# Performance work log

Hardware: AMD Instinct MI355X
Metric: run time of the kernel (lower is better)

Reference implementation:

```python
import math
import jax, jax.numpy as jnp
import numpy as np

HALF_PI = math.pi / 2
TWOR_SCALE = 1.0 / math.log(2.0)
B, C, L, K = 32, 2, 262144, 4


def setup_inputs() -> dict:
    key = jax.random.key(0)
    ks = jax.random.split(key, 6)
    return {
        "input_signal": jax.random.normal(ks[0], (B, C, L), jnp.float32),
        "twoR": jax.random.normal(ks[1], (B, K), jnp.float32),
        "G": jax.random.normal(ks[2], (B, K), jnp.float32),
        "c_hp": jax.random.normal(ks[3], (B, K), jnp.float32),
        "c_bp": jax.random.normal(ks[4], (B, K), jnp.float32),
        "c_lp": jax.random.normal(ks[5], (B, K), jnp.float32),
    }


def get_biquad_coefficients(twoR, G, c_hp, c_bp, c_lp):
    # each arg: (B, K)
    G2 = G * G
    b0 = c_hp + c_bp * G + c_lp * G2
    b1 = -2.0 * c_hp + 2.0 * c_lp * G2
    b2 = c_hp - c_bp * G + c_lp * G2
    a0 = 1.0 + G2 + twoR * G
    a1 = 2.0 * G2 - 2.0
    a2 = 1.0 + G2 - twoR * G
    return jnp.stack([b0, b1, b2], -1), jnp.stack([a0, a1, a2], -1)  # (B,K,3)


def _biquad_cascade(x, Bs, As):
    # x: (B,C,L); Bs, As: (B,1,K,3) -- broadcast over channels.
    # Direct-form II transposed, cascaded in series over K filters.
    Bs = Bs / As[..., :1]
    As = As / As[..., :1]
    b_, c_ = x.shape[0], x.shape[1]
    y = x
    num_filters = Bs.shape[2]
    for k in range(num_filters):
        b0, b1, b2 = Bs[:, :, k, 0], Bs[:, :, k, 1], Bs[:, :, k, 2]  # (B,1)
        a1, a2 = As[:, :, k, 1], As[:, :, k, 2]  # (B,1)

        def step(carry, xt):
            s1, s2 = carry
            yt = b0 * xt + s1              # (B,C)
            s1n = b1 * xt - a1 * yt + s2
            s2n = b2 * xt - a2 * yt
            return (s1n, s2n), yt

        init = (jnp.zeros((b_, c_), y.dtype), jnp.zeros((b_, c_), y.dtype))
        _, yT = jax.lax.scan(step, init, jnp.moveaxis(y, -1, 0))  # (L,B,C)
        y = jnp.moveaxis(yT, 0, -1)
    return y


def reference(input_signal, twoR, G, c_hp, c_bp, c_lp):
    G = jnp.tan(HALF_PI * jax.nn.sigmoid(G))
    twoR = TWOR_SCALE * jax.nn.softplus(twoR) + 0.01
    Bs, As = get_biquad_coefficients(twoR, G, c_hp, c_bp, c_lp)  # (B,K,3)
    Bs, As = Bs[:, None], As[:, None]  # unsqueeze(1): (B,1,K,3)
    return _biquad_cascade(input_signal, Bs, As)
```

## Files before the change

kernel.cpp:

```cpp
#include <hip/hip_runtime.h>
#include <math.h>

#define B_N 32
#define C_N 2
#define L_N 262144
#define K_N 4
#define NSEQ (B_N * C_N)
#define CHUNK 64
#define THREADS 256
#define BLKSAMP (CHUNK * THREADS)
#define NBLK_SEQ (L_N / BLKSAMP)
#define NBLK_TOT (NSEQ * NBLK_SEQ)
#define NLVL 8

#define WS_COEF 0
#define WS_PL   (B_N * 20)
#define WS_PBLK (WS_PL + B_N * 8 * 64)
#define WS_AGG  (WS_PBLK + B_N * 64)
#define WS_SBLK (WS_AGG + NBLK_TOT * 8)

__global__ __launch_bounds__(64) void svf_prep(
    const float* __restrict__ twoR, const float* __restrict__ Graw,
    const float* __restrict__ c_hp, const float* __restrict__ c_bp,
    const float* __restrict__ c_lp, float* __restrict__ ws)
{
    const int b = blockIdx.x;
    const int t = threadIdx.x;
    __shared__ double cf[K_N][5];
    __shared__ double M[8][8];

    if (t < K_N) {
        const int k = t;
        double g  = (double)Graw[b * K_N + k];
        double tr = (double)twoR[b * K_N + k];
        double hp = (double)c_hp[b * K_N + k];
        double bp = (double)c_bp[b * K_N + k];
        double lp = (double)c_lp[b * K_N + k];
        double sg = 1.0 / (1.0 + exp(-g));
        double G  = tan(1.5707963267948966 * sg);
        double R  = log1p(exp(tr)) * 1.4426950408889634 + 0.01;
        double G2 = G * G;
        double b0 = hp + bp * G + lp * G2;
        double b1 = -2.0 * hp + 2.0 * lp * G2;
        double b2 = hp - bp * G + lp * G2;
        double a0 = 1.0 + G2 + R * G;
        double a1 = 2.0 * G2 - 2.0;
        double a2 = 1.0 + G2 - R * G;
        cf[k][0] = b0 / a0; cf[k][1] = b1 / a0; cf[k][2] = b2 / a0;
        cf[k][3] = a1 / a0; cf[k][4] = a2 / a0;
    }
    __syncthreads();

    if (t < 20) ws[WS_COEF + b * 20 + t] = (float)cf[t / 5][t % 5];

    if (t < 8) {
        double s[8];
        #pragma unroll
        for (int i = 0; i < 8; ++i) s[i] = (i == t) ? 1.0 : 0.0;
        double in = 0.0;
        #pragma unroll
        for (int k = 0; k < K_N; ++k) {
            double y   = cf[k][0] * in + s[2 * k];
            double s1n = cf[k][1] * in - cf[k][3] * y + s[2 * k + 1];
            double s2n = cf[k][2] * in - cf[k][4] * y;
            s[2 * k] = s1n; s[2 * k + 1] = s2n; in = y;
        }
        #pragma unroll
        for (int i = 0; i < 8; ++i) M[i][t] = s[i];
    }
    __syncthreads();

    const int i = t >> 3, j = t & 7;
    for (int p = 1; p <= 14; ++p) {
        double acc = 0.0;
        #pragma unroll
        for (int k = 0; k < 8; ++k) acc += M[i][k] * M[k][j];
        __syncthreads();
        M[i][j] = acc;
        __syncthreads();
        if (p >= 6 && p <= 13) ws[WS_PL + (b * 8 + (p - 6)) * 64 + t] = (float)acc;
        if (p == 14)           ws[WS_PBLK + b * 64 + t] = (float)acc;
    }
}

__device__ __forceinline__ float cascade_step(const float cf[20], float s[8], float in)
{
    #pragma unroll
    for (int k = 0; k < K_N; ++k) {
        float y  = fmaf(cf[k * 5 + 0], in, s[2 * k]);
        float t1 = fmaf(cf[k * 5 + 1], in, s[2 * k + 1]);
        float n1 = fmaf(-cf[k * 5 + 3], y, t1);
        float n2 = fmaf(-cf[k * 5 + 4], y, cf[k * 5 + 2] * in);
        s[2 * k] = n1; s[2 * k + 1] = n2;
        in = y;
    }
    return in;
}

__global__ __launch_bounds__(THREADS) void svf_pass1(
    const float* __restrict__ x, const float* __restrict__ ws,
    float* __restrict__ out)
{
    const int seq = blockIdx.x >> 4;
    const int blk = blockIdx.x & (NBLK_SEQ - 1);
    const int tid = threadIdx.x;
    const int b   = seq >> 1;

    __shared__ float Pm[NLVL][64];
    __shared__ float tb[THREADS][9];

    for (int q = tid; q < NLVL * 64; q += THREADS)
        Pm[q >> 6][q & 63] = ws[WS_PL + b * 8 * 64 + q];

    float cf[20];
    #pragma unroll
    for (int q = 0; q < 20; ++q) cf[q] = ws[WS_COEF + b * 20 + q];

    const size_t base = (size_t)seq * L_N + (size_t)blk * BLKSAMP + (size_t)tid * CHUNK;
    const float4* xp = (const float4*)(x + base);
    float t[8] = {0, 0, 0, 0, 0, 0, 0, 0};
    #pragma unroll
    for (int t4 = 0; t4 < CHUNK / 4; ++t4) {
        float4 v = xp[t4];
        (void)cascade_step(cf, t, v.x);
        (void)cascade_step(cf, t, v.y);
        (void)cascade_step(cf, t, v.z);
        (void)cascade_step(cf, t, v.w);
    }
    __syncthreads();

    for (int l = 0; l < NLVL; ++l) {
        const int d = 1 << l;
        #pragma unroll
        for (int q = 0; q < 8; ++q) tb[tid][q] = t[q];
        __syncthreads();
        float prev[8];
        const bool have = (tid >= d);
        if (have) {
            #pragma unroll
            for (int q = 0; q < 8; ++q) prev[q] = tb[tid - d][q];
        }
        __syncthreads();
        if (have) {
            #pragma unroll
            for (int r = 0; r < 8; ++r) {
                float acc = t[r];
                #pragma unroll
                for (int c = 0; c < 8; ++c)
                    acc = fmaf(Pm[l][r * 8 + c], prev[c], acc);
                t[r] = acc;
            }
        }
    }

    #pragma unroll
    for (int q = 0; q < 8; ++q) tb[tid][q] = t[q];
    __syncthreads();

    float e[8];
    if (tid == 0) {
        #pragma unroll
        for (int q = 0; q < 8; ++q) e[q] = 0.0f;
    } else {
        #pragma unroll
        for (int q = 0; q < 8; ++q) e[q] = tb[tid - 1][q];
    }
    float4* eo = (float4*)(out + base);
    eo[0] = make_float4(e[0], e[1], e[2], e[3]);
    eo[1] = make_float4(e[4], e[5], e[6], e[7]);

    if (tid == THREADS - 1) {
        float* agg = (float*)ws + WS_AGG + (size_t)blockIdx.x * 8;
        #pragma unroll
        for (int q = 0; q < 8; ++q) agg[q] = t[q];
    }
}

__global__ __launch_bounds__(64) void svf_scanb(float* __restrict__ ws)
{
    const int seq = threadIdx.x;
    const int b   = seq >> 1;
    float P[64];
    #pragma unroll
    for (int q = 0; q < 64; ++q) P[q] = ws[WS_PBLK + b * 64 + q];

    const float* agg = ws + WS_AGG + (size_t)seq * NBLK_SEQ * 8;
    float* sb        = ws + WS_SBLK + (size_t)seq * NBLK_SEQ * 8;

    float t[8] = {0, 0, 0, 0, 0, 0, 0, 0};
    float f[8];
    #pragma unroll
    for (int q = 0; q < 8; ++q) f[q] = agg[q];

    for (int j = 0; j < NBLK_SEQ; ++j) {
        float fn[8];
        if (j + 1 < NBLK_SEQ) {
            #pragma unroll
            for (int q = 0; q < 8; ++q) fn[q] = agg[(j + 1) * 8 + q];
        }
        #pragma unroll
        for (int q = 0; q < 8; ++q) sb[j * 8 + q] = t[q];
        float nt[8];
        #pragma unroll
        for (int r = 0; r < 8; ++r) {
            float acc = f[r];
            #pragma unroll
            for (int c = 0; c < 8; ++c) acc = fmaf(P[r * 8 + c], t[c], acc);
            nt[r] = acc;
        }
        #pragma unroll
        for (int q = 0; q < 8; ++q) { t[q] = nt[q]; f[q] = fn[q]; }
    }
}

__global__ __launch_bounds__(THREADS) void svf_pass2(
    const float* __restrict__ x, const float* __restrict__ ws,
    float* __restrict__ out)
{
    const int seq = blockIdx.x >> 4;
    const int blk = blockIdx.x & (NBLK_SEQ - 1);
    const int tid = threadIdx.x;
    const int b   = seq >> 1;

    __shared__ float Pm[NLVL][64];
    for (int q = tid; q < NLVL * 64; q += THREADS)
        Pm[q >> 6][q & 63] = ws[WS_PL + b * 8 * 64 + q];

    float cf[20];
    #pragma unroll
    for (int q = 0; q < 20; ++q) cf[q] = ws[WS_COEF + b * 20 + q];

    const float* sbp = ws + WS_SBLK + (size_t)blockIdx.x * 8;
    float v[8];
    #pragma unroll
    for (int q = 0; q < 8; ++q) v[q] = sbp[q];
    __syncthreads();

    #pragma unroll
    for (int l = 0; l < NLVL; ++l) {
        if ((tid >> l) & 1) {
            float nv[8];
            #pragma unroll
            for (int r = 0; r < 8; ++r) {
                float acc = 0.0f;
                #pragma unroll
                for (int c = 0; c < 8; ++c)
                    acc = fmaf(Pm[l][r * 8 + c], v[c], acc);
                nv[r] = acc;
            }
            #pragma unroll
            for (int q = 0; q < 8; ++q) v[q] = nv[q];
        }
    }

    const size_t base = (size_t)seq * L_N + (size_t)blk * BLKSAMP + (size_t)tid * CHUNK;
    const float4* sp = (const float4*)(out + base);
    float4 e0 = sp[0], e1 = sp[1];
    float s[8] = {e0.x + v[0], e0.y + v[1], e0.z + v[2], e0.w + v[3],
                  e1.x + v[4], e1.y + v[5], e1.z + v[6], e1.w + v[7]};

    const float4* xp = (const float4*)(x + base);
    float4* yp = (float4*)(out + base);
    #pragma unroll
    for (int t4 = 0; t4 < CHUNK / 4; ++t4) {
        float4 xv = xp[t4];
        float y0 = cascade_step(cf, s, xv.x);
        float y1 = cascade_step(cf, s, xv.y);
        float y2 = cascade_step(cf, s, xv.z);
        float y3 = cascade_step(cf, s, xv.w);
        yp[t4] = make_float4(y0, y1, y2, y3);
    }
}

extern "C" void kernel_launch(void* const* d_in, const int* in_sizes, int n_in,
                              void* d_out, int out_size, void* d_ws, size_t ws_size,
                              hipStream_t stream)
{
    (void)in_sizes; (void)n_in; (void)out_size; (void)ws_size;
    const float* x    = (const float*)d_in[0];
    const float* twoR = (const float*)d_in[1];
    const float* G    = (const float*)d_in[2];
    const float* chp  = (const float*)d_in[3];
    const float* cbp  = (const float*)d_in[4];
    const float* clp  = (const float*)d_in[5];
    float* out = (float*)d_out;
    float* ws  = (float*)d_ws;

    svf_prep <<<B_N, 64, 0, stream>>>(twoR, G, chp, cbp, clp, ws);
    svf_pass1<<<NBLK_TOT, THREADS, 0, stream>>>(x, ws, out);
    svf_scanb<<<1, 64, 0, stream>>>(ws);
    svf_pass2<<<NBLK_TOT, THREADS, 0, stream>>>(x, ws, out);
}
```

Before: 202.0 us.

## Stage input tiles through padded LDS for coalesced loads and stores; halve block size

Pass1 and pass2 now load each block's input tile cooperatively with coalesced float4 reads into a padded shared-memory array, and each thread runs its 64-sample chunk from LDS. Pass2 writes outputs back to LDS and stores them coalesced. Before, each thread streamed its own contiguous chunk, so a wavefront's accesses were strided by 256 bytes. Threads per block drop to 128, with one fewer scan level and one fewer matrix power. The block scan now reuses the aggregate buffer in place, removing the separate prefix buffer. The cost is about 33KB of LDS per block plus extra barriers, which may limit occupancy.

```diff
diff --git a/kernel.cpp b/kernel.cpp
--- a/kernel.cpp
+++ b/kernel.cpp
@@ -7,17 +7,17 @@
 #define K_N 4
 #define NSEQ (B_N * C_N)
 #define CHUNK 64
-#define THREADS 256
+#define THREADS 128
 #define BLKSAMP (CHUNK * THREADS)
 #define NBLK_SEQ (L_N / BLKSAMP)
 #define NBLK_TOT (NSEQ * NBLK_SEQ)
-#define NLVL 8
+#define NLVL 7
+#define ROWP (CHUNK + 1)
 
 #define WS_COEF 0
 #define WS_PL   (B_N * 20)
-#define WS_PBLK (WS_PL + B_N * 8 * 64)
+#define WS_PBLK (WS_PL + B_N * NLVL * 64)
 #define WS_AGG  (WS_PBLK + B_N * 64)
-#define WS_SBLK (WS_AGG + NBLK_TOT * 8)
 
 __global__ __launch_bounds__(64) void svf_prep(
     const float* __restrict__ twoR, const float* __restrict__ Graw,
@@ -71,15 +71,15 @@
     __syncthreads();
 
     const int i = t >> 3, j = t & 7;
-    for (int p = 1; p <= 14; ++p) {
+    for (int p = 1; p <= 13; ++p) {
         double acc = 0.0;
         #pragma unroll
         for (int k = 0; k < 8; ++k) acc += M[i][k] * M[k][j];
         __syncthreads();
         M[i][j] = acc;
         __syncthreads();
-        if (p >= 6 && p <= 13) ws[WS_PL + (b * 8 + (p - 6)) * 64 + t] = (float)acc;
-        if (p == 14)           ws[WS_PBLK + b * 64 + t] = (float)acc;
+        if (p >= 6 && p <= 12) ws[WS_PL + (b * NLVL + (p - 6)) * 64 + t] = (float)acc;
+        if (p == 13)           ws[WS_PBLK + b * 64 + t] = (float)acc;
     }
 }
 
@@ -97,37 +97,46 @@
     return in;
 }
 
+__device__ __forceinline__ void load_tile(const float* __restrict__ xg,
+                                          float* __restrict__ xt, int tid)
+{
+    #pragma unroll
+    for (int k = 0; k < BLKSAMP / 4 / THREADS; ++k) {
+        const int g0 = (tid + k * THREADS) * 4;
+        float4 v = ((const float4*)xg)[tid + k * THREADS];
+        const int a = (g0 >> 6) * ROWP + (g0 & 63);
+        xt[a] = v.x; xt[a + 1] = v.y; xt[a + 2] = v.z; xt[a + 3] = v.w;
+    }
+}
+
 __global__ __launch_bounds__(THREADS) void svf_pass1(
     const float* __restrict__ x, const float* __restrict__ ws,
     float* __restrict__ out)
 {
-    const int seq = blockIdx.x >> 4;
+    const int seq = blockIdx.x >> 5;
     const int blk = blockIdx.x & (NBLK_SEQ - 1);
     const int tid = threadIdx.x;
     const int b   = seq >> 1;
 
+    __shared__ float xt[THREADS * ROWP];
     __shared__ float Pm[NLVL][64];
     __shared__ float tb[THREADS][9];
 
     for (int q = tid; q < NLVL * 64; q += THREADS)
-        Pm[q >> 6][q & 63] = ws[WS_PL + b * 8 * 64 + q];
+        Pm[q >> 6][q & 63] = ws[WS_PL + b * NLVL * 64 + q];
 
     float cf[20];
     #pragma unroll
     for (int q = 0; q < 20; ++q) cf[q] = ws[WS_COEF + b * 20 + q];
 
-    const size_t base = (size_t)seq * L_N + (size_t)blk * BLKSAMP + (size_t)tid * CHUNK;
-    const float4* xp = (const float4*)(x + base);
+    const size_t base = (size_t)seq * L_N + (size_t)blk * BLKSAMP;
+    load_tile(x + base, xt, tid);
+    __syncthreads();
+
     float t[8] = {0, 0, 0, 0, 0, 0, 0, 0};
-    #pragma unroll
-    for (int t4 = 0; t4 < CHUNK / 4; ++t4) {
-        float4 v = xp[t4];
-        (void)cascade_step(cf, t, v.x);
-        (void)cascade_step(cf, t, v.y);
-        (void)cascade_step(cf, t, v.z);
-        (void)cascade_step(cf, t, v.w);
-    }
-    __syncthreads();
+    const float* xr = &xt[tid * ROWP];
+    #pragma unroll 4
+    for (int j = 0; j < CHUNK; ++j) (void)cascade_step(cf, t, xr[j]);
 
     for (int l = 0; l < NLVL; ++l) {
         const int d = 1 << l;
@@ -153,21 +162,14 @@
         }
     }
 
-    #pragma unroll
-    for (int q = 0; q < 8; ++q) tb[tid][q] = t[q];
-    __syncthreads();
-
-    float e[8];
-    if (tid == 0) {
-        #pragma unroll
-        for (int q = 0; q < 8; ++q) e[q] = 0.0f;
-    } else {
+    float e[8] = {0, 0, 0, 0, 0, 0, 0, 0};
+    if (tid > 0) {
         #pragma unroll
         for (int q = 0; q < 8; ++q) e[q] = tb[tid - 1][q];
     }
     float4* eo = (float4*)(out + base);
-    eo[0] = make_float4(e[0], e[1], e[2], e[3]);
-    eo[1] = make_float4(e[4], e[5], e[6], e[7]);
+    eo[2 * tid]     = make_float4(e[0], e[1], e[2], e[3]);
+    eo[2 * tid + 1] = make_float4(e[4], e[5], e[6], e[7]);
 
     if (tid == THREADS - 1) {
         float* agg = (float*)ws + WS_AGG + (size_t)blockIdx.x * 8;
@@ -184,22 +186,15 @@
     #pragma unroll
     for (int q = 0; q < 64; ++q) P[q] = ws[WS_PBLK + b * 64 + q];
 
-    const float* agg = ws + WS_AGG + (size_t)seq * NBLK_SEQ * 8;
-    float* sb        = ws + WS_SBLK + (size_t)seq * NBLK_SEQ * 8;
+    float* agg = ws + WS_AGG + (size_t)seq * NBLK_SEQ * 8;
 
     float t[8] = {0, 0, 0, 0, 0, 0, 0, 0};
-    float f[8];
-    #pragma unroll
-    for (int q = 0; q < 8; ++q) f[q] = agg[q];
-
     for (int j = 0; j < NBLK_SEQ; ++j) {
-        float fn[8];
-        if (j + 1 < NBLK_SEQ) {
-            #pragma unroll
-            for (int q = 0; q < 8; ++q) fn[q] = agg[(j + 1) * 8 + q];
-        }
-        #pragma unroll
-        for (int q = 0; q < 8; ++q) sb[j * 8 + q] = t[q];
+        float f[8];
+        #pragma unroll
+        for (int q = 0; q < 8; ++q) f[q] = agg[j * 8 + q];
+        #pragma unroll
+        for (int q = 0; q < 8; ++q) agg[j * 8 + q] = t[q];
         float nt[8];
         #pragma unroll
         for (int r = 0; r < 8; ++r) {
@@ -209,7 +204,7 @@
             nt[r] = acc;
         }
         #pragma unroll
-        for (int q = 0; q < 8; ++q) { t[q] = nt[q]; f[q] = fn[q]; }
+        for (int q = 0; q < 8; ++q) t[q] = nt[q];
     }
 }
 
@@ -217,25 +212,34 @@
     const float* __restrict__ x, const float* __restrict__ ws,
     float* __restrict__ out)
 {
-    const int seq = blockIdx.x >> 4;
+    const int seq = blockIdx.x >> 5;
     const int blk = blockIdx.x & (NBLK_SEQ - 1);
     const int tid = threadIdx.x;
     const int b   = seq >> 1;
 
+    __shared__ float xt[THREADS * ROWP];
     __shared__ float Pm[NLVL][64];
+
     for (int q = tid; q < NLVL * 64; q += THREADS)
-        Pm[q >> 6][q & 63] = ws[WS_PL + b * 8 * 64 + q];
+        Pm[q >> 6][q & 63] = ws[WS_PL + b * NLVL * 64 + q];
 
     float cf[20];
     #pragma unroll
     for (int q = 0; q < 20; ++q) cf[q] = ws[WS_COEF + b * 20 + q];
 
-    const float* sbp = ws + WS_SBLK + (size_t)blockIdx.x * 8;
+    const size_t base = (size_t)seq * L_N + (size_t)blk * BLKSAMP;
+
+    const float4* eo = (const float4*)(out + base);
+    float4 e0 = eo[2 * tid], e1 = eo[2 * tid + 1];
+
+    const float* sbp = ws + WS_AGG + (size_t)blockIdx.x * 8;
     float v[8];
     #pragma unroll
     for (int q = 0; q < 8; ++q) v[q] = sbp[q];
-    __syncthreads();
-
+
+    load_tile(x + base, xt, tid);
+
+    __syncthreads();
     #pragma unroll
     for (int l = 0; l < NLVL; ++l) {
         if ((tid >> l) & 1) {
@@ -253,22 +257,20 @@
         }
     }
 
-    const size_t base = (size_t)seq * L_N + (size_t)blk * BLKSAMP + (size_t)tid * CHUNK;
-    const float4* sp = (const float4*)(out + base);
-    float4 e0 = sp[0], e1 = sp[1];
     float s[8] = {e0.x + v[0], e0.y + v[1], e0.z + v[2], e0.w + v[3],
                   e1.x + v[4], e1.y + v[5], e1.z + v[6], e1.w + v[7]};
 
-    const float4* xp = (const float4*)(x + base);
-    float4* yp = (float4*)(out + base);
-    #pragma unroll
-    for (int t4 = 0; t4 < CHUNK / 4; ++t4) {
-        float4 xv = xp[t4];
-        float y0 = cascade_step(cf, s, xv.x);
-        float y1 = cascade_step(cf, s, xv.y);
-        float y2 = cascade_step(cf, s, xv.z);
-        float y3 = cascade_step(cf, s, xv.w);
-        yp[t4] = make_float4(y0, y1, y2, y3);
+    float* xr = &xt[tid * ROWP];
+    #pragma unroll 4
+    for (int j = 0; j < CHUNK; ++j) xr[j] = cascade_step(cf, s, xr[j]);
+    __syncthreads();
+
+    #pragma unroll
+    for (int k = 0; k < BLKSAMP / 4 / THREADS; ++k) {
+        const int g0 = (tid + k * THREADS) * 4;
+        const int a = (g0 >> 6) * ROWP + (g0 & 63);
+        ((float4*)(out + base))[tid + k * THREADS] =
+            make_float4(xt[a], xt[a + 1], xt[a + 2], xt[a + 3]);
     }
 }
 
```

After: 172.6 us. -14.6%, faster.
